# Optimization experiments

Hardware: AMD Instinct MI355X
Metric: run time of the kernel (lower is better)

The kernel has to match this reference:

```python
import jax, jax.numpy as jnp
import numpy as np

B, S, D, H, K, L, NS, NT = 32, 512, 1024, 512, 16, 16, 16, 16
SMOOTH = 0.1
EPS = 1e-8


def setup_inputs() -> dict:
    key = jax.random.key(0)
    ks = jax.random.split(key, 16)
    hidden_layers = jax.random.normal(ks[0], (B, S, D), jnp.float32)
    span_start = jax.random.randint(ks[1], (B, K), 0, S - L).astype(jnp.int32)
    span_idx = span_start[..., None] + jnp.arange(L, dtype=jnp.int32)  # [B,K,L] in-range
    span_mask = jnp.ones((B, K, L), jnp.float32)
    span_end = span_start + (L - 1)
    length = jnp.full((B,), S, jnp.int32)
    slot_emb = jax.random.normal(ks[2], (B, K, D), jnp.float32)
    tgt_slot_embs = jax.random.normal(ks[3], (NT, D), jnp.float32)
    src_slot_ids = jax.random.randint(ks[4], (B, K), 0, NS).astype(jnp.int32)
    sc = 0.02
    p = {
        'Wih_f': jax.random.normal(ks[5], (4 * H, D)) * sc,
        'Whh_f': jax.random.normal(ks[6], (4 * H, H)) * sc,
        'bih_f': jnp.zeros((4 * H,)), 'bhh_f': jnp.zeros((4 * H,)),
        'Wih_b': jax.random.normal(ks[7], (4 * H, D)) * sc,
        'Whh_b': jax.random.normal(ks[8], (4 * H, H)) * sc,
        'bih_b': jnp.zeros((4 * H,)), 'bhh_b': jnp.zeros((4 * H,)),
        # slot_name_projection_for_slot / _for_context are eye-initialized with zero bias
        'Wps1': jnp.eye(D), 'bps1': jnp.zeros((D,)),
        'Wps2': jnp.eye(D), 'bps2': jnp.zeros((D,)),
        'Wpc1': jnp.eye(D), 'bpc1': jnp.zeros((D,)),
        'Wpc2': jnp.eye(D), 'bpc2': jnp.zeros((D,)),
    }
    inp = dict(hidden_layers=hidden_layers, span_idx=span_idx, span_mask=span_mask,
               span_start=span_start, span_end=span_end, length=length,
               slot_emb=slot_emb, tgt_slot_embs=tgt_slot_embs, src_slot_ids=src_slot_ids)
    inp.update(p)
    return inp


def _lstm_dir(x, m, Wih, Whh, bih, bhh):
    # x: [N,L,D], m: [N,L]; masked steps carry state through, emit 0
    N = x.shape[0]
    h0 = jnp.zeros((N, H), x.dtype)
    c0 = jnp.zeros((N, H), x.dtype)

    def step(carry, xm):
        h, c = carry
        xt, mt = xm
        g = xt @ Wih.T + h @ Whh.T + (bih + bhh)
        i, f, gg, o = jnp.split(g, 4, axis=-1)  # torch gate order i,f,g,o
        cn = jax.nn.sigmoid(f) * c + jax.nn.sigmoid(i) * jnp.tanh(gg)
        hn = jax.nn.sigmoid(o) * jnp.tanh(cn)
        mt = mt[:, None]
        h = mt * hn + (1.0 - mt) * h
        c = mt * cn + (1.0 - mt) * c
        return (h, c), h * mt

    _, ys = jax.lax.scan(step, (h0, c0), (jnp.swapaxes(x, 0, 1), m.T))
    return jnp.swapaxes(ys, 0, 1)  # [N,L,H]


def _mlp(x, W1, b1, W2, b2):
    # Linear -> Tanh -> (Dropout eval=identity) -> Linear
    return jnp.tanh(x @ W1.T + b1) @ W2.T + b2


def reference(hidden_layers, span_idx, span_mask, span_start, span_end, length,
              slot_emb, tgt_slot_embs, src_slot_ids,
              Wih_f, Whh_f, bih_f, bhh_f, Wih_b, Whh_b, bih_b, bhh_b,
              Wps1, bps1, Wps2, bps2, Wpc1, bpc1, Wpc2, bpc2):
    # gather span tokens: [B,K,L,D]
    spans = hidden_layers[jnp.arange(B)[:, None, None], span_idx]
    x = spans.reshape(B * K, L, D)
    m = span_mask.reshape(B * K, L)
    hf = _lstm_dir(x, m, Wih_f, Whh_f, bih_f, bhh_f)
    hb = _lstm_dir(x[:, ::-1], m[:, ::-1], Wih_b, Whh_b, bih_b, bhh_b)[:, ::-1]
    out = jnp.concatenate([hf, hb], axis=-1)           # [BK,L,2H]
    slot_feats = out.sum(axis=1).reshape(B, K, 2 * H)  # sum-pool over span

    # context attention (faithful to source: returns attn @ hidden, no softmax)
    sf = jax.lax.stop_gradient(slot_feats)
    pos = jnp.arange(S)
    cmask = (pos[None, None, :] < span_start[..., None]) | \
            ((pos[None, None, :] > span_end[..., None]) & (pos[None, None, :] < length[:, None, None]))
    attn = jnp.einsum('bkd,bsd->bks', sf, hidden_layers) * cmask.astype(hidden_layers.dtype)
    context = jnp.einsum('bks,bsd->bkd', attn, hidden_layers)  # [B,K,D]

    # smooth labels via projected slot-name embeddings (all detached in source)
    s_cat = jnp.concatenate([_mlp(slot_emb, Wps1, bps1, Wps2, bps2),
                             _mlp(slot_emb, Wpc1, bpc1, Wpc2, bpc2)], axis=-1)  # [B,K,2D]
    t_cat = jnp.concatenate([_mlp(tgt_slot_embs, Wps1, bps1, Wps2, bps2),
                             _mlp(tgt_slot_embs, Wpc1, bpc1, Wpc2, bpc2)], axis=-1)  # [NT,2D]
    s_cat = jax.lax.stop_gradient(s_cat)
    t_cat = jax.lax.stop_gradient(t_cat)
    sn = jnp.maximum(jnp.linalg.norm(s_cat, axis=-1), EPS)
    tn = jnp.maximum(jnp.linalg.norm(t_cat, axis=-1), EPS)
    sim = jnp.einsum('bkd,td->bkt', s_cat, t_cat) / (sn[..., None] * tn[None, None, :])
    sim = sim / sim.sum(axis=-1, keepdims=True) * (1.0 - SMOOTH)
    one_hot = jax.nn.one_hot(src_slot_ids, NS, dtype=sim.dtype) * SMOOTH
    labels = jnp.concatenate([one_hot, sim], axis=-1)  # [B,K,NS+NT]

    return jnp.concatenate([slot_feats, context, labels], axis=-1)  # [B,K,2H+D+NS+NT]
```

## Files before the change

### kernel.cpp

```cpp
#include <hip/hip_runtime.h>
#include <cstdio>

#define B_ 32
#define S_ 512
#define D_ 1024
#define H_ 512
#define K_ 16
#define L_ 16
#define NT_ 16
#define NSEQ 512
#define XROWS 8192
#define G4H 2048
#define OUTC 2080
#define MROWS 528

typedef unsigned short u16;
typedef __bf16 bf16x8 __attribute__((ext_vector_type(8)));
typedef float f32x4 __attribute__((ext_vector_type(4)));

__device__ inline u16 f2b(float f) {
  union { float f; unsigned u; } x; x.f = f;
  unsigned r = x.u + 0x7FFFu + ((x.u >> 16) & 1u);
  return (u16)(r >> 16);
}
__device__ inline float b2f(u16 h) {
  union { unsigned u; float f; } c; c.u = ((unsigned)h) << 16;
  return c.f;
}
__device__ inline float sigf(float x) { return 1.0f / (1.0f + expf(-x)); }
__device__ inline float wredsum(float v) {
#pragma unroll
  for (int off = 32; off > 0; off >>= 1) v += __shfl_xor(v, off);
  return v;
}
__device__ inline void gl16(const u16* g, u16* l) {
  __builtin_amdgcn_global_load_lds(
      (const __attribute__((address_space(1))) unsigned int*)g,
      (__attribute__((address_space(3))) unsigned int*)l, 16, 0, 0);
}

__global__ __launch_bounds__(256) void split_kernel(const float* __restrict__ in,
                                                    u16* __restrict__ hi,
                                                    u16* __restrict__ lo, int n) {
  int i = blockIdx.x * 256 + threadIdx.x;
  if (i >= n) return;
  float x = in[i];
  u16 h = f2b(x);
  hi[i] = h;
  lo[i] = f2b(x - b2f(h));
}

__global__ __launch_bounds__(256) void sesplit_kernel(const float* __restrict__ se,
                                                      const float* __restrict__ tg,
                                                      u16* __restrict__ hi,
                                                      u16* __restrict__ lo) {
  int i = blockIdx.x * 256 + threadIdx.x;
  float x = (i < NSEQ * D_) ? se[i] : tg[i - NSEQ * D_];
  u16 h = f2b(x);
  hi[i] = h;
  lo[i] = f2b(x - b2f(h));
}

__global__ __launch_bounds__(256) void split4_kernel(
    const float* __restrict__ s0, const float* __restrict__ s1,
    const float* __restrict__ s2, const float* __restrict__ s3,
    u16* __restrict__ h0, u16* __restrict__ l0,
    u16* __restrict__ h1, u16* __restrict__ l1,
    u16* __restrict__ h2, u16* __restrict__ l2,
    u16* __restrict__ h3, u16* __restrict__ l3) {
  const float* src = blockIdx.y == 0 ? s0 : blockIdx.y == 1 ? s1 : blockIdx.y == 2 ? s2 : s3;
  u16* hi = blockIdx.y == 0 ? h0 : blockIdx.y == 1 ? h1 : blockIdx.y == 2 ? h2 : h3;
  u16* lo = blockIdx.y == 0 ? l0 : blockIdx.y == 1 ? l1 : blockIdx.y == 2 ? l2 : l3;
  int i = blockIdx.x * 256 + threadIdx.x;
  float x = src[i];
  u16 h = f2b(x);
  hi[i] = h;
  lo[i] = f2b(x - b2f(h));
}

__global__ __launch_bounds__(256) void hsplit_kernel(const float* __restrict__ in,
                                                     u16* __restrict__ hi,
                                                     u16* __restrict__ lo) {
  size_t i = ((size_t)blockIdx.x * 256 + threadIdx.x) * 4;
  float4 v = *reinterpret_cast<const float4*>(in + i);
  float a[4] = {v.x, v.y, v.z, v.w};
#pragma unroll
  for (int j = 0; j < 4; ++j) {
    u16 h = f2b(a[j]);
    hi[i + j] = h;
    lo[i + j] = f2b(a[j] - b2f(h));
  }
}

__global__ __launch_bounds__(256) void wprep_kernel(
    const float* __restrict__ Wihf, const float* __restrict__ Wihb,
    const float* __restrict__ Whhf, const float* __restrict__ Whhb,
    u16* __restrict__ Wih2_i, u16* __restrict__ Whhf_i, u16* __restrict__ Whhb_i) {
  int y = blockIdx.y;
  const float* W = y == 0 ? Wihf : y == 1 ? Wihb : y == 2 ? Whhf : Whhb;
  int Kd = (y < 2) ? D_ : H_;
  u16* dst = y == 0 ? Wih2_i : y == 1 ? (Wih2_i + (size_t)G4H * D_) : y == 2 ? Whhf_i : Whhb_i;
  int rp = blockIdx.x;
  int j = rp >> 2, g = rp & 3;
  const float* src = W + ((size_t)(g * H_ + j)) * Kd;
  u16* d = dst + (size_t)rp * Kd;
  for (int k = threadIdx.x; k < Kd; k += 256) d[k] = f2b(src[k]);
}

__global__ __launch_bounds__(256) void bsum2_kernel(
    const float* __restrict__ bihf, const float* __restrict__ bhhf,
    const float* __restrict__ bihb, const float* __restrict__ bhhb,
    float* __restrict__ bsumf, float* __restrict__ bsumb) {
  int i = blockIdx.x * 256 + threadIdx.x;
  int dir = i >> 11;
  int rp = i & (G4H - 1);
  int j = rp >> 2, g = rp & 3;
  const float* bi = dir ? bihb : bihf;
  const float* bh = dir ? bhhb : bhhf;
  float v = bi[g * H_ + j] + bh[g * H_ + j];
  (dir ? bsumb : bsumf)[rp] = v;
}

__global__ __launch_bounds__(256) void big_gemm_kernel(
    const u16* __restrict__ Hh, const int* __restrict__ span_idx,
    const u16* __restrict__ Wih2, u16* __restrict__ G2) {
  __shared__ u16 As[128 * 32];
  __shared__ u16 Bs[128 * 32];
  const int tid = threadIdx.x;
  const int bn = blockIdx.x * 128, bm = blockIdx.y * 128;
  const int wave = tid >> 6, lane = tid & 63;
  const int wm = (wave >> 1) * 64, wn = (wave & 1) * 64;
  const int fr = lane & 15;
  const int kg = (lane >> 4) * 8;

  const u16* asrc[2];
  const u16* bsrc[2];
  u16* adst[2];
  u16* bdst[2];
#pragma unroll
  for (int j = 0; j < 2; ++j) {
    int c = tid + 256 * j;
    int gr = bm + (c >> 2);
    int t = gr >> 9;
    int seq = gr & 511;
    int b = seq >> 4;
    int sidx = span_idx[seq * L_ + t];
    asrc[j] = Hh + ((size_t)(b * S_ + sidx)) * D_ + (c & 3) * 8;
    bsrc[j] = Wih2 + (size_t)(bn + (c >> 2)) * D_ + (c & 3) * 8;
    int ub = (wave * 64 + 256 * j) * 8;
    adst[j] = As + ub;
    bdst[j] = Bs + ub;
  }

  f32x4 acc[4][4] = {};
  for (int k0 = 0; k0 < D_; k0 += 32) {
    gl16(asrc[0] + k0, adst[0]);
    gl16(asrc[1] + k0, adst[1]);
    gl16(bsrc[0] + k0, bdst[0]);
    gl16(bsrc[1] + k0, bdst[1]);
    __syncthreads();
    bf16x8 af[4], bfr[4];
#pragma unroll
    for (int m = 0; m < 4; ++m)
      af[m] = *reinterpret_cast<const bf16x8*>(&As[(wm + m * 16 + fr) * 32 + kg]);
#pragma unroll
    for (int n = 0; n < 4; ++n)
      bfr[n] = *reinterpret_cast<const bf16x8*>(&Bs[(wn + n * 16 + fr) * 32 + kg]);
#pragma unroll
    for (int m = 0; m < 4; ++m)
#pragma unroll
      for (int n = 0; n < 4; ++n)
        acc[m][n] = __builtin_amdgcn_mfma_f32_16x16x32_bf16(af[m], bfr[n], acc[m][n], 0, 0, 0);
    __syncthreads();
  }
  const int ci = lane & 15;
  const int r0 = (lane >> 4) * 4;
#pragma unroll
  for (int m = 0; m < 4; ++m)
#pragma unroll
    for (int n = 0; n < 4; ++n) {
      int col = bn + wn + n * 16 + ci;
#pragma unroll
      for (int r = 0; r < 4; ++r) {
        int row = bm + wm + m * 16 + r0 + r;
        G2[(size_t)row * 4096 + col] = f2b(acc[m][n][r]);
      }
    }
}

__global__ __launch_bounds__(256) void lstm_step_kernel(
    const u16* __restrict__ hbf_in,
    const u16* __restrict__ Whhf, const u16* __restrict__ Whhb,
    const u16* __restrict__ G2,
    const float* __restrict__ bsumf, const float* __restrict__ bsumb,
    const float* __restrict__ mask,
    float* __restrict__ hst, float* __restrict__ cst,
    u16* __restrict__ hbf_out,
    float* __restrict__ sf,
    float* __restrict__ out, u16* __restrict__ sfh, u16* __restrict__ sfl,
    int t, int first, int last) {
  __shared__ u16 As[64 * 32];
  __shared__ u16 Bs[64 * 32];
  const int tid = threadIdx.x;
  const int bz = blockIdx.z;
  const int treal = bz ? (L_ - 1 - t) : t;
  const u16* Whh = bz ? Whhb : Whhf;
  const float* bsum = bz ? bsumb : bsumf;
  const size_t sofs = (size_t)bz * NSEQ * H_;
  const int bm = blockIdx.y * 64, bn = blockIdx.x * 64;
  const int wave = tid >> 6, lane = tid & 63;
  const int wm = (wave >> 1) * 32, wn = (wave & 1) * 32;
  f32x4 acc[2][2] = {};
  const int fr = lane & 15;
  const int kg = (lane >> 4) * 8;

  if (!first) {
    const int c = tid;
    const u16* asrc = hbf_in + sofs + (size_t)(bm + (c >> 2)) * H_ + (c & 3) * 8;
    const u16* bsrc = Whh + (size_t)(bn + (c >> 2)) * H_ + (c & 3) * 8;
    u16* adst = As + wave * 512;
    u16* bdst = Bs + wave * 512;
    for (int k0 = 0; k0 < H_; k0 += 32) {
      gl16(asrc + k0, adst);
      gl16(bsrc + k0, bdst);
      __syncthreads();
      bf16x8 af[2], bfr[2];
#pragma unroll
      for (int m = 0; m < 2; ++m)
        af[m] = *reinterpret_cast<const bf16x8*>(&As[(wm + m * 16 + fr) * 32 + kg]);
#pragma unroll
      for (int n = 0; n < 2; ++n)
        bfr[n] = *reinterpret_cast<const bf16x8*>(&Bs[(wn + n * 16 + fr) * 32 + kg]);
#pragma unroll
      for (int m = 0; m < 2; ++m)
#pragma unroll
        for (int n = 0; n < 2; ++n)
          acc[m][n] = __builtin_amdgcn_mfma_f32_16x16x32_bf16(af[m], bfr[n], acc[m][n], 0, 0, 0);
      __syncthreads();
    }
  }

  const int ci = lane & 15;
  const int r0 = (lane >> 4) * 4;
  const int q = lane & 3;
#pragma unroll
  for (int m = 0; m < 2; ++m)
#pragma unroll
    for (int n = 0; n < 2; ++n) {
      int c = bn + wn + n * 16 + ci;
      int rowbase = bm + wm + m * 16 + r0;
      float val[4];
#pragma unroll
      for (int r = 0; r < 4; ++r) {
        int nrow = rowbase + r;
        float g2 = b2f(G2[((size_t)treal * NSEQ + nrow) * 4096 + (size_t)bz * 2048 + c]);
        val[r] = acc[m][n][r] + g2 + bsum[c];
      }
      float x1[4], x2[4], x3[4];
#pragma unroll
      for (int r = 0; r < 4; ++r) {
        x1[r] = __shfl_xor(val[r], 1);
        x2[r] = __shfl_xor(val[r], 2);
        x3[r] = __shfl_xor(x1[r], 2);
      }
      if (q == 0) {
        int j = c >> 2;
#pragma unroll
        for (int r = 0; r < 4; ++r) {
          int nrow = rowbase + r;
          float gi = val[r], gf = x1[r], gg = x2[r], go = x3[r];
          float mv = mask[nrow * L_ + treal];
          size_t sidx = sofs + (size_t)nrow * H_ + j;
          float co = first ? 0.f : cst[sidx];
          float ho = first ? 0.f : hst[sidx];
          float cn = sigf(gf) * co + sigf(gi) * tanhf(gg);
          float hn = sigf(go) * tanhf(cn);
          float hnew = mv * hn + (1.f - mv) * ho;
          float cnew = mv * cn + (1.f - mv) * co;
          hst[sidx] = hnew;
          cst[sidx] = cnew;
          hbf_out[sidx] = f2b(hnew);
          size_t fidx = (size_t)nrow * 1024 + bz * 512 + j;
          float contrib = hnew * mv;
          float snew = first ? contrib : sf[fidx] + contrib;
          sf[fidx] = snew;
          if (last) {
            out[(size_t)nrow * OUTC + bz * 512 + j] = snew;
            u16 hh = f2b(snew);
            sfh[fidx] = hh;
            sfl[fidx] = f2b(snew - b2f(hh));
          }
        }
      }
    }
}

__global__ __launch_bounds__(256) void attn_mfma_kernel(
    const u16* __restrict__ sfh, const u16* __restrict__ sfl,
    const u16* __restrict__ Hh, const u16* __restrict__ Hl,
    const int* __restrict__ sstart, const int* __restrict__ send,
    const int* __restrict__ len,
    float* __restrict__ attn_f) {
  __shared__ u16 Bh[128 * 32];
  __shared__ u16 Bl[128 * 32];
  const int b = blockIdx.x;
  const int s0 = blockIdx.y * 128;
  const int tid = threadIdx.x;
  const int wave = tid >> 6, lane = tid & 63;
  const int fr = lane & 15;
  const int kg = (lane >> 4) * 8;
  f32x4 acc[2] = {};

  const u16* hsrc[2];
  const u16* lsrc[2];
  u16* hdst[2];
  u16* ldst[2];
#pragma unroll
  for (int j = 0; j < 2; ++j) {
    int c = tid + 256 * j;
    size_t goff = ((size_t)b * S_ + s0 + (c >> 2)) * D_ + (c & 3) * 8;
    hsrc[j] = Hh + goff;
    lsrc[j] = Hl + goff;
    int ub = (wave * 64 + 256 * j) * 8;
    hdst[j] = Bh + ub;
    ldst[j] = Bl + ub;
  }

  for (int k0 = 0; k0 < D_; k0 += 32) {
    gl16(hsrc[0] + k0, hdst[0]);
    gl16(hsrc[1] + k0, hdst[1]);
    gl16(lsrc[0] + k0, ldst[0]);
    gl16(lsrc[1] + k0, ldst[1]);
    __syncthreads();
    size_t aoff = ((size_t)b * 16 + fr) * D_ + k0 + kg;
    bf16x8 ah = *reinterpret_cast<const bf16x8*>(sfh + aoff);
    bf16x8 al = *reinterpret_cast<const bf16x8*>(sfl + aoff);
#pragma unroll
    for (int nt = 0; nt < 2; ++nt) {
      bf16x8 bh = *reinterpret_cast<const bf16x8*>(&Bh[(wave * 32 + nt * 16 + fr) * 32 + kg]);
      bf16x8 bl = *reinterpret_cast<const bf16x8*>(&Bl[(wave * 32 + nt * 16 + fr) * 32 + kg]);
      acc[nt] = __builtin_amdgcn_mfma_f32_16x16x32_bf16(ah, bh, acc[nt], 0, 0, 0);
      acc[nt] = __builtin_amdgcn_mfma_f32_16x16x32_bf16(ah, bl, acc[nt], 0, 0, 0);
      acc[nt] = __builtin_amdgcn_mfma_f32_16x16x32_bf16(al, bh, acc[nt], 0, 0, 0);
    }
    __syncthreads();
  }
  const int ln = len[b];
#pragma unroll
  for (int nt = 0; nt < 2; ++nt) {
    int s = s0 + wave * 32 + nt * 16 + (lane & 15);
#pragma unroll
    for (int r = 0; r < 4; ++r) {
      int krow = (lane >> 4) * 4 + r;
      int bk = b * 16 + krow;
      int st = sstart[bk], en = send[bk];
      bool cm = (s < st) || ((s > en) && (s < ln));
      attn_f[(size_t)bk * S_ + s] = cm ? acc[nt][r] : 0.f;
    }
  }
}

__global__ __launch_bounds__(256) void ctx_f32_kernel(
    const float* __restrict__ attn_f, const float* __restrict__ hidden,
    float* __restrict__ out) {
  __shared__ float att[16 * 512];
  const int b = blockIdx.x;
  const int d0 = blockIdx.y * 128;
  const int tid = threadIdx.x;
  for (int i = tid; i < 16 * 512; i += 256)
    att[i] = attn_f[((size_t)b * 16 + (i >> 9)) * S_ + (i & 511)];
  __syncthreads();
  const int d = d0 + (tid & 127);
  const int sh = tid >> 7;
  float acc[16] = {};
  const float* hp = hidden + ((size_t)b * S_ + sh * 256) * D_ + d;
  for (int s = 0; s < 256; ++s) {
    float hv = hp[(size_t)s * D_];
    int si = sh * 256 + s;
#pragma unroll
    for (int kr = 0; kr < 16; ++kr) acc[kr] += att[kr * 512 + si] * hv;
  }
  __syncthreads();
  float* red = att;
#pragma unroll
  for (int kr = 0; kr < 16; ++kr) red[(sh * 16 + kr) * 128 + (tid & 127)] = acc[kr];
  __syncthreads();
  if (sh == 0) {
#pragma unroll
    for (int kr = 0; kr < 16; ++kr)
      out[((size_t)b * 16 + kr) * OUTC + 1024 + d] =
          red[kr * 128 + (tid & 127)] + red[(16 + kr) * 128 + (tid & 127)];
  }
}

__global__ __launch_bounds__(256) void mlp_gemm_kernel(
    const u16* __restrict__ Ah, const u16* __restrict__ Al, int a_br_stride,
    const u16* __restrict__ B0h, const u16* __restrict__ B0l,
    const u16* __restrict__ B1h, const u16* __restrict__ B1l,
    float* __restrict__ P, int M) {
  __shared__ u16 Ash[64 * 32];
  __shared__ u16 Asl[64 * 32];
  __shared__ u16 Bsh[64 * 32];
  __shared__ u16 Bsl[64 * 32];
  const int tid = threadIdx.x;
  const int zz = blockIdx.z;
  const int br = zz >> 2, ks = zz & 3;
  const u16* Ah_ = Ah + (size_t)br * a_br_stride;
  const u16* Al_ = Al + (size_t)br * a_br_stride;
  const u16* Bh = br ? B1h : B0h;
  const u16* Bl = br ? B1l : B0l;
  const int bm = blockIdx.y * 64, bn = blockIdx.x * 64;
  const int wave = tid >> 6, lane = tid & 63;
  const int wm = (wave >> 1) * 32, wn = (wave & 1) * 32;
  f32x4 acc[2][2] = {};
  const int fr = lane & 15;
  const int kg = (lane >> 4) * 8;

  const int c = tid;
  int ga = bm + (c >> 2);
  if (ga >= M) ga = M - 1;
  const u16* ahsrc = Ah_ + (size_t)ga * D_ + (c & 3) * 8;
  const u16* alsrc = Al_ + (size_t)ga * D_ + (c & 3) * 8;
  const u16* bhsrc = Bh + (size_t)(bn + (c >> 2)) * D_ + (c & 3) * 8;
  const u16* blsrc = Bl + (size_t)(bn + (c >> 2)) * D_ + (c & 3) * 8;
  u16* d0 = Ash + wave * 512;
  u16* d1 = Asl + wave * 512;
  u16* d2 = Bsh + wave * 512;
  u16* d3 = Bsl + wave * 512;

  const int kbeg = ks * 256;
  for (int k0 = kbeg; k0 < kbeg + 256; k0 += 32) {
    gl16(ahsrc + k0, d0);
    gl16(alsrc + k0, d1);
    gl16(bhsrc + k0, d2);
    gl16(blsrc + k0, d3);
    __syncthreads();
    bf16x8 afh[2], afl[2], bfh[2], bfl[2];
#pragma unroll
    for (int m = 0; m < 2; ++m) {
      afh[m] = *reinterpret_cast<const bf16x8*>(&Ash[(wm + m * 16 + fr) * 32 + kg]);
      afl[m] = *reinterpret_cast<const bf16x8*>(&Asl[(wm + m * 16 + fr) * 32 + kg]);
    }
#pragma unroll
    for (int n = 0; n < 2; ++n) {
      bfh[n] = *reinterpret_cast<const bf16x8*>(&Bsh[(wn + n * 16 + fr) * 32 + kg]);
      bfl[n] = *reinterpret_cast<const bf16x8*>(&Bsl[(wn + n * 16 + fr) * 32 + kg]);
    }
#pragma unroll
    for (int m = 0; m < 2; ++m)
#pragma unroll
      for (int n = 0; n < 2; ++n) {
        acc[m][n] = __builtin_amdgcn_mfma_f32_16x16x32_bf16(afh[m], bfh[n], acc[m][n], 0, 0, 0);
        acc[m][n] = __builtin_amdgcn_mfma_f32_16x16x32_bf16(afh[m], bfl[n], acc[m][n], 0, 0, 0);
        acc[m][n] = __builtin_amdgcn_mfma_f32_16x16x32_bf16(afl[m], bfh[n], acc[m][n], 0, 0, 0);
      }
    __syncthreads();
  }
  const int ci = lane & 15;
  const int r0 = (lane >> 4) * 4;
#pragma unroll
  for (int m = 0; m < 2; ++m)
#pragma unroll
    for (int n = 0; n < 2; ++n) {
      int col = bn + wn + n * 16 + ci;
#pragma unroll
      for (int r = 0; r < 4; ++r) {
        int row = bm + wm + m * 16 + r0 + r;
        if (row < M)
          P[((size_t)zz * MROWS + row) * D_ + col] = acc[m][n][r];
      }
    }
}

__global__ __launch_bounds__(256) void mlp_reduce_kernel(
    const float* __restrict__ P,
    const float* __restrict__ bias0, const float* __restrict__ bias1,
    u16* __restrict__ Oh, u16* __restrict__ Ol,
    float* __restrict__ Cf,
    int mode) {
  int i = blockIdx.x * 256 + threadIdx.x;
  int e = i * 4;
  const int per_br = MROWS * D_;
  int br = e / per_br;
  int rem = e - br * per_br;
  int row = rem >> 10;
  int col = rem & 1023;
  float4 s = {0.f, 0.f, 0.f, 0.f};
#pragma unroll
  for (int ks = 0; ks < 4; ++ks) {
    float4 v = *reinterpret_cast<const float4*>(
        P + ((size_t)(br * 4 + ks) * MROWS + row) * D_ + col);
    s.x += v.x; s.y += v.y; s.z += v.z; s.w += v.w;
  }
  const float* bias = br ? bias1 : bias0;
  s.x += bias[col]; s.y += bias[col + 1]; s.z += bias[col + 2]; s.w += bias[col + 3];
  if (mode == 0) {
    float a[4] = {tanhf(s.x), tanhf(s.y), tanhf(s.z), tanhf(s.w)};
    size_t o = (size_t)br * per_br + (size_t)row * D_ + col;
#pragma unroll
    for (int j = 0; j < 4; ++j) {
      u16 h = f2b(a[j]);
      Oh[o + j] = h;
      Ol[o + j] = f2b(a[j] - b2f(h));
    }
  } else {
    *reinterpret_cast<float4*>(Cf + (size_t)row * 2048 + br * 1024 + col) = s;
  }
}

__global__ __launch_bounds__(64) void labels_kernel(
    const float* __restrict__ s_cat, const float* __restrict__ t_cat,
    const int* __restrict__ src_ids, float* __restrict__ out) {
  int bk = blockIdx.x, lane = threadIdx.x;
  const float* srow = s_cat + (size_t)bk * 2048;
  float np = 0.f;
  float dots[16], tsq[16];
#pragma unroll
  for (int t = 0; t < 16; ++t) { dots[t] = 0.f; tsq[t] = 0.f; }
  for (int j = lane; j < 2048; j += 64) {
    float sv = srow[j];
    np += sv * sv;
#pragma unroll
    for (int t = 0; t < 16; ++t) {
      float tv = t_cat[t * 2048 + j];
      dots[t] += sv * tv;
      tsq[t] += tv * tv;
    }
  }
  np = wredsum(np);
#pragma unroll
  for (int t = 0; t < 16; ++t) { dots[t] = wredsum(dots[t]); tsq[t] = wredsum(tsq[t]); }
  float sn = fmaxf(sqrtf(np), 1e-8f);
  float ssum = 0.f;
  float sims[16];
#pragma unroll
  for (int t = 0; t < 16; ++t) {
    float tn = fmaxf(sqrtf(tsq[t]), 1e-8f);
    sims[t] = dots[t] / (sn * tn);
    ssum += sims[t];
  }
  float scale = 0.9f / ssum;
  if (lane < 16) {
    out[(size_t)bk * OUTC + 2064 + lane] = sims[lane] * scale;
  } else if (lane < 32) {
    int t2 = lane - 16;
    out[(size_t)bk * OUTC + 2048 + t2] = (src_ids[bk] == t2) ? 0.1f : 0.f;
  }
}

extern "C" void kernel_launch(void* const* d_in, const int* in_sizes, int n_in,
                              void* d_out, int out_size, void* d_ws, size_t ws_size,
                              hipStream_t stream) {
  const float* hidden    = (const float*)d_in[0];
  const int*   span_idx  = (const int*)d_in[1];
  const float* span_mask = (const float*)d_in[2];
  const int*   span_start= (const int*)d_in[3];
  const int*   span_end  = (const int*)d_in[4];
  const int*   length    = (const int*)d_in[5];
  const float* slot_emb  = (const float*)d_in[6];
  const float* tgt       = (const float*)d_in[7];
  const int*   src_ids   = (const int*)d_in[8];
  const float* Wih_f = (const float*)d_in[9];
  const float* Whh_f = (const float*)d_in[10];
  const float* bih_f = (const float*)d_in[11];
  const float* bhh_f = (const float*)d_in[12];
  const float* Wih_b = (const float*)d_in[13];
  const float* Whh_b = (const float*)d_in[14];
  const float* bih_b = (const float*)d_in[15];
  const float* bhh_b = (const float*)d_in[16];
  const float* Wps1 = (const float*)d_in[17];
  const float* bps1 = (const float*)d_in[18];
  const float* Wps2 = (const float*)d_in[19];
  const float* bps2 = (const float*)d_in[20];
  const float* Wpc1 = (const float*)d_in[21];
  const float* bpc1 = (const float*)d_in[22];
  const float* Wpc2 = (const float*)d_in[23];
  const float* bpc2 = (const float*)d_in[24];
  float* out = (float*)d_out;

  char* p = (char*)d_ws;
  auto alloc = [&](size_t bytes) -> void* {
    void* r = (void*)p;
    p += (bytes + 255) & ~(size_t)255;
    return r;
  };
  char*  BIG1  = (char*)alloc((size_t)XROWS * 4096 * 2);
  char*  BIG2  = (char*)alloc((size_t)2 * B_ * S_ * D_ * 2);
  float* hst   = (float*)alloc((size_t)2 * NSEQ * H_ * 4);
  float* cst   = (float*)alloc((size_t)2 * NSEQ * H_ * 4);
  u16*   hbfA  = (u16*)alloc((size_t)2 * NSEQ * H_ * 2);
  u16*   hbfB  = (u16*)alloc((size_t)2 * NSEQ * H_ * 2);
  float* sf    = (float*)alloc((size_t)NSEQ * 1024 * 4);
  u16*   sfh   = (u16*)alloc((size_t)NSEQ * 1024 * 2);
  u16*   sfl   = (u16*)alloc((size_t)NSEQ * 1024 * 2);
  float* attn_f= (float*)alloc((size_t)NSEQ * S_ * 4);
  float* CAT   = (float*)alloc((size_t)MROWS * 2048 * 4);
  u16* Wih2_i = (u16*)alloc((size_t)2 * G4H * D_ * 2);
  u16* Whhf_i = (u16*)alloc((size_t)G4H * H_ * 2);
  u16* Whhb_i = (u16*)alloc((size_t)G4H * H_ * 2);
  float* bsumf = (float*)alloc(G4H * 4);
  float* bsumb = (float*)alloc(G4H * 4);
  u16* W1sh = (u16*)alloc((size_t)D_ * D_ * 2); u16* W1sl = (u16*)alloc((size_t)D_ * D_ * 2);
  u16* W2sh = (u16*)alloc((size_t)D_ * D_ * 2); u16* W2sl = (u16*)alloc((size_t)D_ * D_ * 2);
  u16* W1ch = (u16*)alloc((size_t)D_ * D_ * 2); u16* W1cl = (u16*)alloc((size_t)D_ * D_ * 2);
  u16* W2ch = (u16*)alloc((size_t)D_ * D_ * 2); u16* W2cl = (u16*)alloc((size_t)D_ * D_ * 2);
  u16* SEh = (u16*)alloc((size_t)MROWS * D_ * 2); u16* SEl = (u16*)alloc((size_t)MROWS * D_ * 2);
  u16* T1h = (u16*)alloc((size_t)2 * MROWS * D_ * 2);
  u16* T1l = (u16*)alloc((size_t)2 * MROWS * D_ * 2);

  u16*   G2 = (u16*)BIG1;
  float* P  = (float*)BIG1;
  u16*   Hh = (u16*)BIG2;
  u16*   Hl = Hh + (size_t)B_ * S_ * D_;

  size_t need = (size_t)(p - (char*)d_ws);
  if (need > ws_size) {
    fprintf(stderr, "kernel_launch: ws too small, need %zu have %zu\n", need, ws_size);
    return;
  }

  {
    dim3 g(G4H, 4);
    wprep_kernel<<<g, 256, 0, stream>>>(Wih_f, Wih_b, Whh_f, Whh_b,
                                        Wih2_i, Whhf_i, Whhb_i);
  }
  bsum2_kernel<<<(2 * G4H) / 256, 256, 0, stream>>>(bih_f, bhh_f, bih_b, bhh_b,
                                                    bsumf, bsumb);
  {
    dim3 g((D_ * D_) / 256, 4);
    split4_kernel<<<g, 256, 0, stream>>>(Wps1, Wps2, Wpc1, Wpc2,
                                         W1sh, W1sl, W2sh, W2sl,
                                         W1ch, W1cl, W2ch, W2cl);
  }
  sesplit_kernel<<<(MROWS * D_) / 256, 256, 0, stream>>>(slot_emb, tgt, SEh, SEl);

  hsplit_kernel<<<(B_ * S_ * D_) / (4 * 256), 256, 0, stream>>>(hidden, Hh, Hl);

  {
    dim3 g(4096 / 128, XROWS / 128);
    big_gemm_kernel<<<g, 256, 0, stream>>>(Hh, span_idx, Wih2_i, G2);
  }

  for (int t = 0; t < L_; ++t) {
    const u16* hin = (t & 1) ? hbfA : hbfB;
    u16* hout = (t & 1) ? hbfB : hbfA;
    dim3 g(G4H / 64, NSEQ / 64, 2);
    lstm_step_kernel<<<g, 256, 0, stream>>>(hin, Whhf_i, Whhb_i, G2, bsumf, bsumb,
                                            span_mask, hst, cst, hout, sf,
                                            out, sfh, sfl,
                                            t, t == 0 ? 1 : 0, t == L_ - 1 ? 1 : 0);
  }

  {
    dim3 g(B_, S_ / 128);
    attn_mfma_kernel<<<g, 256, 0, stream>>>(sfh, sfl, Hh, Hl,
                                            span_start, span_end, length, attn_f);
  }
  {
    dim3 g(B_, D_ / 128);
    ctx_f32_kernel<<<g, 256, 0, stream>>>(attn_f, hidden, out);
  }

  {
    dim3 g(D_ / 64, (MROWS + 63) / 64, 8);
    dim3 rg((2 * MROWS * D_) / (4 * 256));
    mlp_gemm_kernel<<<g, 256, 0, stream>>>(SEh, SEl, 0, W1sh, W1sl, W1ch, W1cl, P, MROWS);
    mlp_reduce_kernel<<<rg, 256, 0, stream>>>(P, bps1, bpc1, T1h, T1l, nullptr, 0);
    mlp_gemm_kernel<<<g, 256, 0, stream>>>(T1h, T1l, MROWS * D_, W2sh, W2sl, W2ch, W2cl, P, MROWS);
    mlp_reduce_kernel<<<rg, 256, 0, stream>>>(P, bps2, bpc2, nullptr, nullptr, CAT, 1);
  }

  const float* t_cat = CAT + (size_t)NSEQ * 2048;
  labels_kernel<<<NSEQ, 64, 0, stream>>>(CAT, t_cat, src_ids, out);
}
```

Measured before the change: 639.9 us.

## Double-buffer LDS tiles in GEMM kernels and vectorize context accumulation

```diff
diff --git a/kernel.cpp b/kernel.cpp
--- a/kernel.cpp
+++ b/kernel.cpp
@@ -38,6 +38,7 @@
       (const __attribute__((address_space(1))) unsigned int*)g,
       (__attribute__((address_space(3))) unsigned int*)l, 16, 0, 0);
 }
+#define VMCNT(N) asm volatile("s_waitcnt vmcnt(" #N ")" ::: "memory")
 
 __global__ __launch_bounds__(256) void split_kernel(const float* __restrict__ in,
                                                     u16* __restrict__ hi,
@@ -124,8 +125,8 @@
 __global__ __launch_bounds__(256) void big_gemm_kernel(
     const u16* __restrict__ Hh, const int* __restrict__ span_idx,
     const u16* __restrict__ Wih2, u16* __restrict__ G2) {
-  __shared__ u16 As[128 * 32];
-  __shared__ u16 Bs[128 * 32];
+  __shared__ u16 As[2][128 * 32];
+  __shared__ u16 Bs[2][128 * 32];
   const int tid = threadIdx.x;
   const int bn = blockIdx.x * 128, bm = blockIdx.y * 128;
   const int wave = tid >> 6, lane = tid & 63;
@@ -135,8 +136,7 @@
 
   const u16* asrc[2];
   const u16* bsrc[2];
-  u16* adst[2];
-  u16* bdst[2];
+  int doff[2];
 #pragma unroll
   for (int j = 0; j < 2; ++j) {
     int c = tid + 256 * j;
@@ -147,32 +147,50 @@
     int sidx = span_idx[seq * L_ + t];
     asrc[j] = Hh + ((size_t)(b * S_ + sidx)) * D_ + (c & 3) * 8;
     bsrc[j] = Wih2 + (size_t)(bn + (c >> 2)) * D_ + (c & 3) * 8;
-    int ub = (wave * 64 + 256 * j) * 8;
-    adst[j] = As + ub;
-    bdst[j] = Bs + ub;
+    doff[j] = (j * 256 + wave * 64) * 8;
   }
 
   f32x4 acc[4][4] = {};
-  for (int k0 = 0; k0 < D_; k0 += 32) {
-    gl16(asrc[0] + k0, adst[0]);
-    gl16(asrc[1] + k0, adst[1]);
-    gl16(bsrc[0] + k0, bdst[0]);
-    gl16(bsrc[1] + k0, bdst[1]);
-    __syncthreads();
+  auto STAGE = [&](int buf, int k0) {
+    gl16(asrc[0] + k0, &As[buf][doff[0]]);
+    gl16(asrc[1] + k0, &As[buf][doff[1]]);
+    gl16(bsrc[0] + k0, &Bs[buf][doff[0]]);
+    gl16(bsrc[1] + k0, &Bs[buf][doff[1]]);
+  };
+  auto COMPUTE = [&](int buf) {
     bf16x8 af[4], bfr[4];
 #pragma unroll
     for (int m = 0; m < 4; ++m)
-      af[m] = *reinterpret_cast<const bf16x8*>(&As[(wm + m * 16 + fr) * 32 + kg]);
+      af[m] = *reinterpret_cast<const bf16x8*>(&As[buf][(wm + m * 16 + fr) * 32 + kg]);
 #pragma unroll
     for (int n = 0; n < 4; ++n)
-      bfr[n] = *reinterpret_cast<const bf16x8*>(&Bs[(wn + n * 16 + fr) * 32 + kg]);
+      bfr[n] = *reinterpret_cast<const bf16x8*>(&Bs[buf][(wn + n * 16 + fr) * 32 + kg]);
 #pragma unroll
     for (int m = 0; m < 4; ++m)
 #pragma unroll
       for (int n = 0; n < 4; ++n)
         acc[m][n] = __builtin_amdgcn_mfma_f32_16x16x32_bf16(af[m], bfr[n], acc[m][n], 0, 0, 0);
-    __syncthreads();
-  }
+  };
+
+  STAGE(0, 0);
+  STAGE(1, 32);
+  for (int k = 0; k < D_; k += 64) {
+    VMCNT(4);
+    __builtin_amdgcn_s_barrier();
+    COMPUTE(0);
+    __builtin_amdgcn_s_barrier();
+    if (k + 64 < D_) {
+      STAGE(0, k + 64);
+      VMCNT(4);
+    } else {
+      VMCNT(0);
+    }
+    __builtin_amdgcn_s_barrier();
+    COMPUTE(1);
+    __builtin_amdgcn_s_barrier();
+    if (k + 96 < D_) STAGE(1, k + 96);
+  }
+
   const int ci = lane & 15;
   const int r0 = (lane >> 4) * 4;
 #pragma unroll
@@ -199,8 +217,8 @@
     float* __restrict__ sf,
     float* __restrict__ out, u16* __restrict__ sfh, u16* __restrict__ sfl,
     int t, int first, int last) {
-  __shared__ u16 As[64 * 32];
-  __shared__ u16 Bs[64 * 32];
+  __shared__ u16 As[2][64 * 32];
+  __shared__ u16 Bs[2][64 * 32];
   const int tid = threadIdx.x;
   const int bz = blockIdx.z;
   const int treal = bz ? (L_ - 1 - t) : t;
@@ -218,25 +236,42 @@
     const int c = tid;
     const u16* asrc = hbf_in + sofs + (size_t)(bm + (c >> 2)) * H_ + (c & 3) * 8;
     const u16* bsrc = Whh + (size_t)(bn + (c >> 2)) * H_ + (c & 3) * 8;
-    u16* adst = As + wave * 512;
-    u16* bdst = Bs + wave * 512;
-    for (int k0 = 0; k0 < H_; k0 += 32) {
-      gl16(asrc + k0, adst);
-      gl16(bsrc + k0, bdst);
-      __syncthreads();
+    const int doff = wave * 512;
+    auto STAGE = [&](int buf, int k0) {
+      gl16(asrc + k0, &As[buf][doff]);
+      gl16(bsrc + k0, &Bs[buf][doff]);
+    };
+    auto COMPUTE = [&](int buf) {
       bf16x8 af[2], bfr[2];
 #pragma unroll
       for (int m = 0; m < 2; ++m)
-        af[m] = *reinterpret_cast<const bf16x8*>(&As[(wm + m * 16 + fr) * 32 + kg]);
+        af[m] = *reinterpret_cast<const bf16x8*>(&As[buf][(wm + m * 16 + fr) * 32 + kg]);
 #pragma unroll
       for (int n = 0; n < 2; ++n)
-        bfr[n] = *reinterpret_cast<const bf16x8*>(&Bs[(wn + n * 16 + fr) * 32 + kg]);
+        bfr[n] = *reinterpret_cast<const bf16x8*>(&Bs[buf][(wn + n * 16 + fr) * 32 + kg]);
 #pragma unroll
       for (int m = 0; m < 2; ++m)
 #pragma unroll
         for (int n = 0; n < 2; ++n)
           acc[m][n] = __builtin_amdgcn_mfma_f32_16x16x32_bf16(af[m], bfr[n], acc[m][n], 0, 0, 0);
-      __syncthreads();
+    };
+    STAGE(0, 0);
+    STAGE(1, 32);
+    for (int k = 0; k < H_; k += 64) {
+      VMCNT(2);
+      __builtin_amdgcn_s_barrier();
+      COMPUTE(0);
+      __builtin_amdgcn_s_barrier();
+      if (k + 64 < H_) {
+        STAGE(0, k + 64);
+        VMCNT(2);
+      } else {
+        VMCNT(0);
+      }
+      __builtin_amdgcn_s_barrier();
+      COMPUTE(1);
+      __builtin_amdgcn_s_barrier();
+      if (k + 96 < H_) STAGE(1, k + 96);
     }
   }
 
@@ -374,11 +409,17 @@
   const int sh = tid >> 7;
   float acc[16] = {};
   const float* hp = hidden + ((size_t)b * S_ + sh * 256) * D_ + d;
-  for (int s = 0; s < 256; ++s) {
-    float hv = hp[(size_t)s * D_];
-    int si = sh * 256 + s;
-#pragma unroll
-    for (int kr = 0; kr < 16; ++kr) acc[kr] += att[kr * 512 + si] * hv;
+  for (int s4 = 0; s4 < 64; ++s4) {
+    float h0 = hp[(size_t)(s4 * 4 + 0) * D_];
+    float h1 = hp[(size_t)(s4 * 4 + 1) * D_];
+    float h2 = hp[(size_t)(s4 * 4 + 2) * D_];
+    float h3 = hp[(size_t)(s4 * 4 + 3) * D_];
+    int si = sh * 256 + s4 * 4;
+#pragma unroll
+    for (int kr = 0; kr < 16; ++kr) {
+      float4 a4 = *reinterpret_cast<const float4*>(&att[kr * 512 + si]);
+      acc[kr] += a4.x * h0 + a4.y * h1 + a4.z * h2 + a4.w * h3;
+    }
   }
   __syncthreads();
   float* red = att;
@@ -398,10 +439,10 @@
     const u16* __restrict__ B0h, const u16* __restrict__ B0l,
     const u16* __restrict__ B1h, const u16* __restrict__ B1l,
     float* __restrict__ P, int M) {
-  __shared__ u16 Ash[64 * 32];
-  __shared__ u16 Asl[64 * 32];
-  __shared__ u16 Bsh[64 * 32];
-  __shared__ u16 Bsl[64 * 32];
+  __shared__ u16 Ash[2][64 * 32];
+  __shared__ u16 Asl[2][64 * 32];
+  __shared__ u16 Bsh[2][64 * 32];
+  __shared__ u16 Bsl[2][64 * 32];
   const int tid = threadIdx.x;
   const int zz = blockIdx.z;
   const int br = zz >> 2, ks = zz & 3;
@@ -423,28 +464,25 @@
   const u16* alsrc = Al_ + (size_t)ga * D_ + (c & 3) * 8;
   const u16* bhsrc = Bh + (size_t)(bn + (c >> 2)) * D_ + (c & 3) * 8;
   const u16* blsrc = Bl + (size_t)(bn + (c >> 2)) * D_ + (c & 3) * 8;
-  u16* d0 = Ash + wave * 512;
-  u16* d1 = Asl + wave * 512;
-  u16* d2 = Bsh + wave * 512;
-  u16* d3 = Bsl + wave * 512;
-
-  const int kbeg = ks * 256;
-  for (int k0 = kbeg; k0 < kbeg + 256; k0 += 32) {
-    gl16(ahsrc + k0, d0);
-    gl16(alsrc + k0, d1);
-    gl16(bhsrc + k0, d2);
-    gl16(blsrc + k0, d3);
-    __syncthreads();
+  const int doff = wave * 512;
+
+  auto STAGE = [&](int buf, int k0) {
+    gl16(ahsrc + k0, &Ash[buf][doff]);
+    gl16(alsrc + k0, &Asl[buf][doff]);
+    gl16(bhsrc + k0, &Bsh[buf][doff]);
+    gl16(blsrc + k0, &Bsl[buf][doff]);
+  };
+  auto COMPUTE = [&](int buf) {
     bf16x8 afh[2], afl[2], bfh[2], bfl[2];
 #pragma unroll
     for (int m = 0; m < 2; ++m) {
-      afh[m] = *reinterpret_cast<const bf16x8*>(&Ash[(wm + m * 16 + fr) * 32 + kg]);
-      afl[m] = *reinterpret_cast<const bf16x8*>(&Asl[(wm + m * 16 + fr) * 32 + kg]);
+      afh[m] = *reinterpret_cast<const bf16x8*>(&Ash[buf][(wm + m * 16 + fr) * 32 + kg]);
+      afl[m] = *reinterpret_cast<const bf16x8*>(&Asl[buf][(wm + m * 16 + fr) * 32 + kg]);
     }
 #pragma unroll
     for (int n = 0; n < 2; ++n) {
-      bfh[n] = *reinterpret_cast<const bf16x8*>(&Bsh[(wn + n * 16 + fr) * 32 + kg]);
-      bfl[n] = *reinterpret_cast<const bf16x8*>(&Bsl[(wn + n * 16 + fr) * 32 + kg]);
+      bfh[n] = *reinterpret_cast<const bf16x8*>(&Bsh[buf][(wn + n * 16 + fr) * 32 + kg]);
+      bfl[n] = *reinterpret_cast<const bf16x8*>(&Bsl[buf][(wn + n * 16 + fr) * 32 + kg]);
     }
 #pragma unroll
     for (int m = 0; m < 2; ++m)
@@ -454,7 +492,27 @@
         acc[m][n] = __builtin_amdgcn_mfma_f32_16x16x32_bf16(afh[m], bfl[n], acc[m][n], 0, 0, 0);
         acc[m][n] = __builtin_amdgcn_mfma_f32_16x16x32_bf16(afl[m], bfh[n], acc[m][n], 0, 0, 0);
       }
-    __syncthreads();
+  };
+
+  const int kbeg = ks * 256;
+  const int kend = kbeg + 256;
+  STAGE(0, kbeg);
+  STAGE(1, kbeg + 32);
+  for (int k = kbeg; k < kend; k += 64) {
+    VMCNT(4);
+    __builtin_amdgcn_s_barrier();
+    COMPUTE(0);
+    __builtin_amdgcn_s_barrier();
+    if (k + 64 < kend) {
+      STAGE(0, k + 64);
+      VMCNT(4);
+    } else {
+      VMCNT(0);
+    }
+    __builtin_amdgcn_s_barrier();
+    COMPUTE(1);
+    __builtin_amdgcn_s_barrier();
+    if (k + 96 < kend) STAGE(1, k + 96);
   }
   const int ci = lane & 15;
   const int r0 = (lane >> 4) * 4;
```

Measured after the change: 637.4 us. About the same (-0.4%).

## Fuse LSTM steps into one cooperative kernel and merge prep kernels

Applied to the files above, without the earlier changes.

```diff
diff --git a/kernel.cpp b/kernel.cpp
--- a/kernel.cpp
+++ b/kernel.cpp
@@ -1,5 +1,8 @@
 #include <hip/hip_runtime.h>
+#include <hip/hip_cooperative_groups.h>
 #include <cstdio>
+
+namespace cg = cooperative_groups;
 
 #define B_ 32
 #define S_ 512
@@ -39,86 +42,86 @@
       (__attribute__((address_space(3))) unsigned int*)l, 16, 0, 0);
 }
 
-__global__ __launch_bounds__(256) void split_kernel(const float* __restrict__ in,
-                                                    u16* __restrict__ hi,
-                                                    u16* __restrict__ lo, int n) {
-  int i = blockIdx.x * 256 + threadIdx.x;
-  if (i >= n) return;
-  float x = in[i];
-  u16 h = f2b(x);
-  hi[i] = h;
-  lo[i] = f2b(x - b2f(h));
-}
-
-__global__ __launch_bounds__(256) void sesplit_kernel(const float* __restrict__ se,
-                                                      const float* __restrict__ tg,
-                                                      u16* __restrict__ hi,
-                                                      u16* __restrict__ lo) {
-  int i = blockIdx.x * 256 + threadIdx.x;
-  float x = (i < NSEQ * D_) ? se[i] : tg[i - NSEQ * D_];
-  u16 h = f2b(x);
-  hi[i] = h;
-  lo[i] = f2b(x - b2f(h));
-}
-
-__global__ __launch_bounds__(256) void split4_kernel(
-    const float* __restrict__ s0, const float* __restrict__ s1,
-    const float* __restrict__ s2, const float* __restrict__ s3,
-    u16* __restrict__ h0, u16* __restrict__ l0,
-    u16* __restrict__ h1, u16* __restrict__ l1,
-    u16* __restrict__ h2, u16* __restrict__ l2,
-    u16* __restrict__ h3, u16* __restrict__ l3) {
-  const float* src = blockIdx.y == 0 ? s0 : blockIdx.y == 1 ? s1 : blockIdx.y == 2 ? s2 : s3;
-  u16* hi = blockIdx.y == 0 ? h0 : blockIdx.y == 1 ? h1 : blockIdx.y == 2 ? h2 : h3;
-  u16* lo = blockIdx.y == 0 ? l0 : blockIdx.y == 1 ? l1 : blockIdx.y == 2 ? l2 : l3;
-  int i = blockIdx.x * 256 + threadIdx.x;
-  float x = src[i];
-  u16 h = f2b(x);
-  hi[i] = h;
-  lo[i] = f2b(x - b2f(h));
-}
-
-__global__ __launch_bounds__(256) void hsplit_kernel(const float* __restrict__ in,
-                                                     u16* __restrict__ hi,
-                                                     u16* __restrict__ lo) {
-  size_t i = ((size_t)blockIdx.x * 256 + threadIdx.x) * 4;
-  float4 v = *reinterpret_cast<const float4*>(in + i);
-  float a[4] = {v.x, v.y, v.z, v.w};
-#pragma unroll
-  for (int j = 0; j < 4; ++j) {
-    u16 h = f2b(a[j]);
-    hi[i + j] = h;
-    lo[i + j] = f2b(a[j] - b2f(h));
-  }
-}
-
-__global__ __launch_bounds__(256) void wprep_kernel(
-    const float* __restrict__ Wihf, const float* __restrict__ Wihb,
-    const float* __restrict__ Whhf, const float* __restrict__ Whhb,
-    u16* __restrict__ Wih2_i, u16* __restrict__ Whhf_i, u16* __restrict__ Whhb_i) {
-  int y = blockIdx.y;
-  const float* W = y == 0 ? Wihf : y == 1 ? Wihb : y == 2 ? Whhf : Whhb;
-  int Kd = (y < 2) ? D_ : H_;
-  u16* dst = y == 0 ? Wih2_i : y == 1 ? (Wih2_i + (size_t)G4H * D_) : y == 2 ? Whhf_i : Whhb_i;
-  int rp = blockIdx.x;
-  int j = rp >> 2, g = rp & 3;
-  const float* src = W + ((size_t)(g * H_ + j)) * Kd;
-  u16* d = dst + (size_t)rp * Kd;
-  for (int k = threadIdx.x; k < Kd; k += 256) d[k] = f2b(src[k]);
-}
-
-__global__ __launch_bounds__(256) void bsum2_kernel(
-    const float* __restrict__ bihf, const float* __restrict__ bhhf,
-    const float* __restrict__ bihb, const float* __restrict__ bhhb,
+#define NB_HS 16384
+#define NB_S4 16384
+#define NB_WP 8192
+#define NB_SE 2112
+__global__ __launch_bounds__(256) void prep_kernel(
+    const float* __restrict__ hidden,
+    const float* __restrict__ Wps1, const float* __restrict__ Wps2,
+    const float* __restrict__ Wpc1, const float* __restrict__ Wpc2,
+    const float* __restrict__ slot_emb, const float* __restrict__ tgt,
+    const float* __restrict__ Wih_f, const float* __restrict__ Wih_b,
+    const float* __restrict__ Whh_f, const float* __restrict__ Whh_b,
+    const float* __restrict__ bih_f, const float* __restrict__ bhh_f,
+    const float* __restrict__ bih_b, const float* __restrict__ bhh_b,
+    u16* __restrict__ Hh, u16* __restrict__ Hl,
+    u16* __restrict__ W1sh, u16* __restrict__ W1sl,
+    u16* __restrict__ W2sh, u16* __restrict__ W2sl,
+    u16* __restrict__ W1ch, u16* __restrict__ W1cl,
+    u16* __restrict__ W2ch, u16* __restrict__ W2cl,
+    u16* __restrict__ SEh, u16* __restrict__ SEl,
+    u16* __restrict__ Wih2_i, u16* __restrict__ Whhf_i, u16* __restrict__ Whhb_i,
     float* __restrict__ bsumf, float* __restrict__ bsumb) {
-  int i = blockIdx.x * 256 + threadIdx.x;
-  int dir = i >> 11;
-  int rp = i & (G4H - 1);
-  int j = rp >> 2, g = rp & 3;
-  const float* bi = dir ? bihb : bihf;
-  const float* bh = dir ? bhhb : bhhf;
-  float v = bi[g * H_ + j] + bh[g * H_ + j];
-  (dir ? bsumb : bsumf)[rp] = v;
+  int bid = blockIdx.x;
+  if (bid < NB_HS) {
+    size_t i = ((size_t)bid * 256 + threadIdx.x) * 4;
+    float4 v = *reinterpret_cast<const float4*>(hidden + i);
+    float a[4] = {v.x, v.y, v.z, v.w};
+#pragma unroll
+    for (int j = 0; j < 4; ++j) {
+      u16 h = f2b(a[j]);
+      Hh[i + j] = h;
+      Hl[i + j] = f2b(a[j] - b2f(h));
+    }
+    return;
+  }
+  bid -= NB_HS;
+  if (bid < NB_S4) {
+    int y = bid >> 12, bx = bid & 4095;
+    const float* src = y == 0 ? Wps1 : y == 1 ? Wps2 : y == 2 ? Wpc1 : Wpc2;
+    u16* hi = y == 0 ? W1sh : y == 1 ? W2sh : y == 2 ? W1ch : W2ch;
+    u16* lo = y == 0 ? W1sl : y == 1 ? W2sl : y == 2 ? W1cl : W2cl;
+    int i = bx * 256 + threadIdx.x;
+    float x = src[i];
+    u16 h = f2b(x);
+    hi[i] = h;
+    lo[i] = f2b(x - b2f(h));
+    return;
+  }
+  bid -= NB_S4;
+  if (bid < NB_WP) {
+    int y = bid >> 11, rp = bid & 2047;
+    const float* W = y == 0 ? Wih_f : y == 1 ? Wih_b : y == 2 ? Whh_f : Whh_b;
+    int Kd = (y < 2) ? D_ : H_;
+    u16* dst = y == 0 ? Wih2_i : y == 1 ? (Wih2_i + (size_t)G4H * D_)
+                               : y == 2 ? Whhf_i : Whhb_i;
+    int j = rp >> 2, g = rp & 3;
+    const float* src = W + ((size_t)(g * H_ + j)) * Kd;
+    u16* d = dst + (size_t)rp * Kd;
+    for (int k = threadIdx.x; k < Kd; k += 256) d[k] = f2b(src[k]);
+    return;
+  }
+  bid -= NB_WP;
+  if (bid < NB_SE) {
+    int i = bid * 256 + threadIdx.x;
+    float x = (i < NSEQ * D_) ? slot_emb[i] : tgt[i - NSEQ * D_];
+    u16 h = f2b(x);
+    SEh[i] = h;
+    SEl[i] = f2b(x - b2f(h));
+    return;
+  }
+  bid -= NB_SE;
+  {
+    int i = bid * 256 + threadIdx.x;
+    int dir = i >> 11;
+    int rp = i & (G4H - 1);
+    int j = rp >> 2, g = rp & 3;
+    const float* bi = dir ? bih_b : bih_f;
+    const float* bh = dir ? bhh_b : bhh_f;
+    float v = bi[g * H_ + j] + bh[g * H_ + j];
+    (dir ? bsumb : bsumf)[rp] = v;
+  }
 }
 
 __global__ __launch_bounds__(256) void big_gemm_kernel(
@@ -185,6 +188,125 @@
         int row = bm + wm + m * 16 + r0 + r;
         G2[(size_t)row * 4096 + col] = f2b(acc[m][n][r]);
       }
+    }
+}
+
+__global__ __launch_bounds__(256) void lstm_seq_kernel(
+    u16* __restrict__ hbf0, u16* __restrict__ hbf1,
+    const u16* __restrict__ Whhf, const u16* __restrict__ Whhb,
+    const u16* __restrict__ G2,
+    const float* __restrict__ bsumf, const float* __restrict__ bsumb,
+    const float* __restrict__ mask,
+    float* __restrict__ out, u16* __restrict__ sfh, u16* __restrict__ sfl) {
+  __shared__ u16 As[64 * 32];
+  __shared__ u16 Bs[64 * 32];
+  cg::grid_group gridg = cg::this_grid();
+  const int tid = threadIdx.x;
+  const int bz = blockIdx.z;
+  const u16* Whh = bz ? Whhb : Whhf;
+  const float* bsum = bz ? bsumb : bsumf;
+  const size_t sofs = (size_t)bz * NSEQ * H_;
+  const int bm = blockIdx.y * 64, bn = blockIdx.x * 64;
+  const int wave = tid >> 6, lane = tid & 63;
+  const int wm = (wave >> 1) * 32, wn = (wave & 1) * 32;
+  const int fr = lane & 15;
+  const int kg = (lane >> 4) * 8;
+  const int ci = lane & 15;
+  const int r0 = (lane >> 4) * 4;
+  const int q = lane & 3;
+
+  const size_t a_fix = sofs + (size_t)(bm + (tid >> 2)) * H_ + (tid & 3) * 8;
+  const u16* bsrc = Whh + (size_t)(bn + (tid >> 2)) * H_ + (tid & 3) * 8;
+  u16* adst = As + wave * 512;
+  u16* bdst = Bs + wave * 512;
+
+  float bsv[2];
+#pragma unroll
+  for (int n = 0; n < 2; ++n) bsv[n] = bsum[bn + wn + n * 16 + ci];
+
+  float hreg[2][2] = {}, creg[2][2] = {}, sfacc[2][2] = {};
+
+  for (int t = 0; t < L_; ++t) {
+    const int treal = bz ? (L_ - 1 - t) : t;
+    f32x4 acc[2][2] = {};
+    if (t > 0) {
+      const u16* hbf_in = (t & 1) ? hbf1 : hbf0;
+      const u16* asrc = hbf_in + a_fix;
+      for (int k0 = 0; k0 < H_; k0 += 32) {
+        gl16(asrc + k0, adst);
+        gl16(bsrc + k0, bdst);
+        __syncthreads();
+        bf16x8 af[2], bfr[2];
+#pragma unroll
+        for (int m = 0; m < 2; ++m)
+          af[m] = *reinterpret_cast<const bf16x8*>(&As[(wm + m * 16 + fr) * 32 + kg]);
+#pragma unroll
+        for (int n = 0; n < 2; ++n)
+          bfr[n] = *reinterpret_cast<const bf16x8*>(&Bs[(wn + n * 16 + fr) * 32 + kg]);
+#pragma unroll
+        for (int m = 0; m < 2; ++m)
+#pragma unroll
+          for (int n = 0; n < 2; ++n)
+            acc[m][n] = __builtin_amdgcn_mfma_f32_16x16x32_bf16(af[m], bfr[n], acc[m][n], 0, 0, 0);
+        __syncthreads();
+      }
+    }
+    u16* hbf_out = (t & 1) ? hbf0 : hbf1;
+#pragma unroll
+    for (int m = 0; m < 2; ++m)
+#pragma unroll
+      for (int n = 0; n < 2; ++n) {
+        int c = bn + wn + n * 16 + ci;
+        int rowbase = bm + wm + m * 16 + r0;
+        float val[4], x1[4], x2[4], x3[4];
+#pragma unroll
+        for (int r = 0; r < 4; ++r) {
+          val[r] = acc[m][n][r] +
+                   b2f(G2[((size_t)treal * NSEQ + rowbase + r) * 4096 + (size_t)bz * 2048 + c]) +
+                   bsv[n];
+          x1[r] = __shfl_xor(val[r], 1);
+          x2[r] = __shfl_xor(val[r], 2);
+          x3[r] = __shfl_xor(x1[r], 2);
+        }
+        auto sel4 = [&](const float v[4]) {
+          float r01 = (q & 1) ? v[1] : v[0];
+          float r23 = (q & 1) ? v[3] : v[2];
+          return (q & 2) ? r23 : r01;
+        };
+        float A0 = sel4(val), A1 = sel4(x1), A2 = sel4(x2), A3 = sel4(x3);
+        float gi = (q & 2) ? ((q & 1) ? A3 : A2) : ((q & 1) ? A1 : A0);
+        float gf = (q & 2) ? ((q & 1) ? A2 : A3) : ((q & 1) ? A0 : A1);
+        float gg = (q & 2) ? ((q & 1) ? A1 : A0) : ((q & 1) ? A3 : A2);
+        float go = (q & 2) ? ((q & 1) ? A0 : A1) : ((q & 1) ? A2 : A3);
+        int nrow = rowbase + q;
+        int j = c >> 2;
+        float mv = mask[nrow * L_ + treal];
+        float co = creg[m][n], ho = hreg[m][n];
+        float cn = sigf(gf) * co + sigf(gi) * tanhf(gg);
+        float hn = sigf(go) * tanhf(cn);
+        float hnew = mv * hn + (1.f - mv) * ho;
+        float cnew = mv * cn + (1.f - mv) * co;
+        hreg[m][n] = hnew;
+        creg[m][n] = cnew;
+        hbf_out[sofs + (size_t)nrow * H_ + j] = f2b(hnew);
+        sfacc[m][n] += hnew * mv;
+      }
+    __threadfence();
+    gridg.sync();
+  }
+#pragma unroll
+  for (int m = 0; m < 2; ++m)
+#pragma unroll
+    for (int n = 0; n < 2; ++n) {
+      int c = bn + wn + n * 16 + ci;
+      int j = c >> 2;
+      int nrow = bm + wm + m * 16 + r0 + q;
+      float snew = sfacc[m][n];
+      size_t fidx = (size_t)nrow * 1024 + bz * 512 + j;
+      out[(size_t)nrow * OUTC + bz * 512 + j] = snew;
+      u16 hh = f2b(snew);
+      sfh[fidx] = hh;
+      sfl[fidx] = f2b(snew - b2f(hh));
     }
 }
 
@@ -374,11 +496,17 @@
   const int sh = tid >> 7;
   float acc[16] = {};
   const float* hp = hidden + ((size_t)b * S_ + sh * 256) * D_ + d;
-  for (int s = 0; s < 256; ++s) {
-    float hv = hp[(size_t)s * D_];
-    int si = sh * 256 + s;
-#pragma unroll
-    for (int kr = 0; kr < 16; ++kr) acc[kr] += att[kr * 512 + si] * hv;
+  for (int s4 = 0; s4 < 64; ++s4) {
+    float h0 = hp[(size_t)(s4 * 4 + 0) * D_];
+    float h1 = hp[(size_t)(s4 * 4 + 1) * D_];
+    float h2 = hp[(size_t)(s4 * 4 + 2) * D_];
+    float h3 = hp[(size_t)(s4 * 4 + 3) * D_];
+    int si = sh * 256 + s4 * 4;
+#pragma unroll
+    for (int kr = 0; kr < 16; ++kr) {
+      float4 a4 = *reinterpret_cast<const float4*>(&att[kr * 512 + si]);
+      acc[kr] += a4.x * h0 + a4.y * h1 + a4.z * h2 + a4.w * h3;
+    }
   }
   __syncthreads();
   float* red = att;
@@ -620,35 +748,38 @@
   }
 
   {
-    dim3 g(G4H, 4);
-    wprep_kernel<<<g, 256, 0, stream>>>(Wih_f, Wih_b, Whh_f, Whh_b,
-                                        Wih2_i, Whhf_i, Whhb_i);
-  }
-  bsum2_kernel<<<(2 * G4H) / 256, 256, 0, stream>>>(bih_f, bhh_f, bih_b, bhh_b,
-                                                    bsumf, bsumb);
-  {
-    dim3 g((D_ * D_) / 256, 4);
-    split4_kernel<<<g, 256, 0, stream>>>(Wps1, Wps2, Wpc1, Wpc2,
-                                         W1sh, W1sl, W2sh, W2sl,
-                                         W1ch, W1cl, W2ch, W2cl);
-  }
-  sesplit_kernel<<<(MROWS * D_) / 256, 256, 0, stream>>>(slot_emb, tgt, SEh, SEl);
-
-  hsplit_kernel<<<(B_ * S_ * D_) / (4 * 256), 256, 0, stream>>>(hidden, Hh, Hl);
+    dim3 g(NB_HS + NB_S4 + NB_WP + NB_SE + 16);
+    prep_kernel<<<g, 256, 0, stream>>>(
+        hidden, Wps1, Wps2, Wpc1, Wpc2, slot_emb, tgt,
+        Wih_f, Wih_b, Whh_f, Whh_b, bih_f, bhh_f, bih_b, bhh_b,
+        Hh, Hl, W1sh, W1sl, W2sh, W2sl, W1ch, W1cl, W2ch, W2cl,
+        SEh, SEl, Wih2_i, Whhf_i, Whhb_i, bsumf, bsumb);
+  }
 
   {
     dim3 g(4096 / 128, XROWS / 128);
     big_gemm_kernel<<<g, 256, 0, stream>>>(Hh, span_idx, Wih2_i, G2);
   }
 
-  for (int t = 0; t < L_; ++t) {
-    const u16* hin = (t & 1) ? hbfA : hbfB;
-    u16* hout = (t & 1) ? hbfB : hbfA;
-    dim3 g(G4H / 64, NSEQ / 64, 2);
-    lstm_step_kernel<<<g, 256, 0, stream>>>(hin, Whhf_i, Whhb_i, G2, bsumf, bsumb,
-                                            span_mask, hst, cst, hout, sf,
-                                            out, sfh, sfl,
-                                            t, t == 0 ? 1 : 0, t == L_ - 1 ? 1 : 0);
+  {
+    dim3 cgrid(G4H / 64, NSEQ / 64, 2);
+    dim3 cblock(256);
+    void* kargs[] = {
+        (void*)&hbfA, (void*)&hbfB, (void*)&Whhf_i, (void*)&Whhb_i,
+        (void*)&G2, (void*)&bsumf, (void*)&bsumb, (void*)&span_mask,
+        (void*)&out, (void*)&sfh, (void*)&sfl};
+    hipError_t ce = hipLaunchCooperativeKernel((void*)lstm_seq_kernel,
+                                               cgrid, cblock, kargs, 0, stream);
+    if (ce != hipSuccess) {
+      for (int t = 0; t < L_; ++t) {
+        const u16* hin = (t & 1) ? hbfA : hbfB;
+        u16* hout = (t & 1) ? hbfB : hbfA;
+        lstm_step_kernel<<<cgrid, 256, 0, stream>>>(
+            hin, Whhf_i, Whhb_i, G2, bsumf, bsumb, span_mask,
+            hst, cst, hout, sf, out, sfh, sfl,
+            t, t == 0 ? 1 : 0, t == L_ - 1 ? 1 : 0);
+      }
+    }
   }
 
   {
```

New measurement: 2.285 ms. 3.57x slower.
